# Performance work log

Hardware: AMD Instinct MI355X
Metric: run time of the kernel (lower is better)

The kernel has to match this reference:

```python
import jax, jax.numpy as jnp
import numpy as np

N_NODES = 100000


def gcn_conv(x, row, col, W, b, n_nodes):
    # PyG GCNConv: add self-loops, symmetric normalization, linear, scatter-add, bias
    deg = jnp.zeros((n_nodes,), x.dtype).at[col].add(1.0)
    dinv = jnp.where(deg > 0, jax.lax.rsqrt(deg), 0.0)
    norm = dinv[row] * dinv[col]                      # [E+N]
    h = x @ W                                         # [N, out]
    msg = h[row] * norm[:, None]                      # [E+N, out]
    out = jax.ops.segment_sum(msg, col, num_segments=n_nodes)
    return out + b


def setup_inputs() -> dict:
    key = jax.random.key(0)
    ks = jax.random.split(key, 8)
    E = 1600000
    edge_index = jax.random.randint(ks[0], (2, E), 0, N_NODES, dtype=jnp.int64)
    node_features = jax.random.normal(ks[1], (N_NODES, 16), dtype=jnp.float32)
    W1 = jax.random.normal(ks[2], (16, 32), dtype=jnp.float32) * 0.25
    b1 = jnp.zeros((32,), jnp.float32)
    W2 = jax.random.normal(ks[3], (32, 16), dtype=jnp.float32) * 0.18
    b2 = jnp.zeros((16,), jnp.float32)
    fc_W = jax.random.normal(ks[4], (16, 1), dtype=jnp.float32) * 0.25
    fc_b = jnp.zeros((1,), jnp.float32)
    return {"edge_index": edge_index, "node_features": node_features,
            "W1": W1, "b1": b1, "W2": W2, "b2": b2, "fc_W": fc_W, "fc_b": fc_b}


def reference(edge_index, node_features, W1, b1, W2, b2, fc_W, fc_b):
    n = node_features.shape[0]
    loops = jnp.arange(n, dtype=edge_index.dtype)
    row = jnp.concatenate([edge_index[0], loops])     # sources (with self-loops)
    col = jnp.concatenate([edge_index[1], loops])     # targets (with self-loops)
    x = jax.nn.relu(gcn_conv(node_features, row, col, W1, b1, n))
    # F.dropout with training=False is identity (inference)
    x = jax.nn.relu(gcn_conv(x, row, col, W2, b2, n))
    return x @ fc_W + fc_b
```

## Files before the change

kernel.cpp:

```cpp
#include <hip/hip_runtime.h>
#include <hip/hip_fp16.h>


constexpr int NN  = 100000;
constexpr int FIN = 16;
constexpr int FH  = 32;
constexpr int FO  = 16;

constexpr int BK      = 256;
constexpr int NBUCKET = (NN + BK - 1) / BK;
constexpr int CHUNK   = 8192;
constexpr int CAP     = 5376;

static __device__ __forceinline__ int pack2(float a, float b) {
    __half2 t = __float22half2_rn(make_float2(a, b));
    return *reinterpret_cast<int*>(&t);
}
static __device__ __forceinline__ float2 unpack2(int v) {
    __half2 t = *reinterpret_cast<__half2*>(&v);
    return __half22float2(t);
}

__global__ void init_kernel(int* __restrict__ bcursor) {
    int b = blockIdx.x * blockDim.x + threadIdx.x;
    if (b < NBUCKET) bcursor[b] = b * CAP;
}

__global__ __launch_bounds__(256) void bucket_fill_kernel(
        const int* __restrict__ row, const int* __restrict__ col,
        int* __restrict__ bcursor, int* __restrict__ srow, int E) {
    __shared__ int bcnt[NBUCKET];
    __shared__ int bcur[NBUCKET];
    int t = threadIdx.x;
    int e0 = blockIdx.x * CHUNK;
    int m = E - e0; if (m > CHUNK) m = CHUNK;
    for (int b = t; b < NBUCKET; b += 256) bcnt[b] = 0;
    __syncthreads();
    for (int i = t; i < m; i += 256)
        atomicAdd(&bcnt[col[e0 + i] >> 8], 1);
    __syncthreads();
    for (int b = t; b < NBUCKET; b += 256) {
        int v = bcnt[b];
        bcur[b] = v ? atomicAdd(&bcursor[b], v) : 0;
    }
    __syncthreads();
    for (int i = t; i < m; i += 256) {
        int c = col[e0 + i];
        int r = row[e0 + i];
        int p = atomicAdd(&bcur[c >> 8], 1);
        srow[p] = ((c & (BK - 1)) << 17) | r;
    }
}

__global__ __launch_bounds__(256) void bucket_sort_mm1_kernel(
        const int* __restrict__ bcursor, int* __restrict__ srow,
        int* __restrict__ off, int* __restrict__ cnt, float* __restrict__ dinv,
        const float* __restrict__ x, const float* __restrict__ W1,
        __half* __restrict__ g1, int n) {
    __shared__ int ebuf[CAP];
    __shared__ int sorted[CAP];
    __shared__ int cnt2[BK];
    __shared__ int aux[BK];
    __shared__ float w1[FIN * FH];
    int t = threadIdx.x;
    for (int i = t; i < FIN * FH; i += 256) w1[i] = W1[i];
    int lo = blockIdx.x << 8;
    int nodes = n - lo; if (nodes > BK) nodes = BK;
    int s0 = blockIdx.x * CAP;
    int m = bcursor[blockIdx.x] - s0;
    if (m > CAP) m = CAP;
    for (int i = t; i < m; i += 256) ebuf[i] = srow[s0 + i];
    cnt2[t] = 0;
    __syncthreads();
    for (int i = t; i < m; i += 256) atomicAdd(&cnt2[ebuf[i] >> 17], 1);
    __syncthreads();
    int v = cnt2[t];
    aux[t] = v;
    __syncthreads();
    for (int d = 1; d < BK; d <<= 1) {
        int a = (t >= d) ? aux[t - d] : 0;
        __syncthreads();
        aux[t] += a;
        __syncthreads();
    }
    int excl = aux[t] - v;
    cnt2[t] = excl;
    float di = rsqrtf((float)v + 1.0f);
    if (t < nodes) {
        off[lo + t]  = s0 + excl;
        cnt[lo + t]  = v;
        dinv[lo + t] = di;
    }
    __syncthreads();
    for (int i = t; i < m; i += 256) {
        int pv = ebuf[i];
        int p = atomicAdd(&cnt2[pv >> 17], 1);
        sorted[p] = pv & 0x1FFFF;
    }
    __syncthreads();
    for (int i = t; i < m; i += 256) srow[s0 + i] = sorted[i];
    if (t < nodes) {
        int nd = lo + t;
        float xi[FIN];
        const float4* xv = (const float4*)(x + (long long)nd * FIN);
        #pragma unroll
        for (int i = 0; i < FIN / 4; i++) {
            float4 vv = xv[i];
            xi[4*i] = vv.x; xi[4*i+1] = vv.y; xi[4*i+2] = vv.z; xi[4*i+3] = vv.w;
        }
        float h[FH];
        #pragma unroll
        for (int j = 0; j < FH; j++) h[j] = 0.f;
        #pragma unroll
        for (int i = 0; i < FIN; i++) {
            float xs = xi[i];
            #pragma unroll
            for (int j = 0; j < FH; j++) h[j] += xs * w1[i * FH + j];
        }
        int4* gv = (int4*)(g1 + (long long)nd * FH);
        #pragma unroll
        for (int k = 0; k < 4; k++) {
            gv[k] = make_int4(pack2(h[8*k]*di,   h[8*k+1]*di),
                              pack2(h[8*k+2]*di, h[8*k+3]*di),
                              pack2(h[8*k+4]*di, h[8*k+5]*di),
                              pack2(h[8*k+6]*di, h[8*k+7]*di));
        }
    }
}

constexpr int XS = 36;
__global__ __launch_bounds__(256) void gather_mm2_kernel(
        const int* __restrict__ off, const int* __restrict__ cnt,
        const int* __restrict__ srow, const __half* __restrict__ g1,
        const float* __restrict__ dinv, const float* __restrict__ b1,
        const float* __restrict__ W2, __half* __restrict__ g2, int n) {
    __shared__ float xs[64 * XS];
    __shared__ float w[FH * FO];
    __shared__ float bb[FH];
    int t = threadIdx.x;
    for (int i = t; i < FH * FO; i += 256) w[i] = W2[i];
    if (t < FH) bb[t] = b1[t];
    int nl = t >> 2;
    int q = t & 3;
    int node = blockIdx.x * 64 + nl;
    bool live = node < n;
    float acc[8] = {0.f,0.f,0.f,0.f,0.f,0.f,0.f,0.f};
    float di = 0.f;
    if (live) {
        di = dinv[node];
        {
            int4 raw = ((const int4*)(g1 + (long long)node * FH))[q];
            float2 f0 = unpack2(raw.x), f1 = unpack2(raw.y);
            float2 f2 = unpack2(raw.z), f3 = unpack2(raw.w);
            acc[0] = f0.x; acc[1] = f0.y; acc[2] = f1.x; acc[3] = f1.y;
            acc[4] = f2.x; acc[5] = f2.y; acc[6] = f3.x; acc[7] = f3.y;
        }
        int s = off[node];
        int m = cnt[node];
        int i = 0;
        for (; i + 3 < m; i += 4) {
            int r0 = srow[s + i];
            int r1 = srow[s + i + 1];
            int r2 = srow[s + i + 2];
            int r3 = srow[s + i + 3];
            int4 ra = ((const int4*)(g1 + (long long)r0 * FH))[q];
            int4 rb = ((const int4*)(g1 + (long long)r1 * FH))[q];
            int4 rc = ((const int4*)(g1 + (long long)r2 * FH))[q];
            int4 rd = ((const int4*)(g1 + (long long)r3 * FH))[q];
            float2 u;
            u = unpack2(ra.x); acc[0] += u.x; acc[1] += u.y;
            u = unpack2(ra.y); acc[2] += u.x; acc[3] += u.y;
            u = unpack2(ra.z); acc[4] += u.x; acc[5] += u.y;
            u = unpack2(ra.w); acc[6] += u.x; acc[7] += u.y;
            u = unpack2(rb.x); acc[0] += u.x; acc[1] += u.y;
            u = unpack2(rb.y); acc[2] += u.x; acc[3] += u.y;
            u = unpack2(rb.z); acc[4] += u.x; acc[5] += u.y;
            u = unpack2(rb.w); acc[6] += u.x; acc[7] += u.y;
            u = unpack2(rc.x); acc[0] += u.x; acc[1] += u.y;
            u = unpack2(rc.y); acc[2] += u.x; acc[3] += u.y;
            u = unpack2(rc.z); acc[4] += u.x; acc[5] += u.y;
            u = unpack2(rc.w); acc[6] += u.x; acc[7] += u.y;
            u = unpack2(rd.x); acc[0] += u.x; acc[1] += u.y;
            u = unpack2(rd.y); acc[2] += u.x; acc[3] += u.y;
            u = unpack2(rd.z); acc[4] += u.x; acc[5] += u.y;
            u = unpack2(rd.w); acc[6] += u.x; acc[7] += u.y;
        }
        for (; i < m; i++) {
            int r0 = srow[s + i];
            int4 ra = ((const int4*)(g1 + (long long)r0 * FH))[q];
            float2 u;
            u = unpack2(ra.x); acc[0] += u.x; acc[1] += u.y;
            u = unpack2(ra.y); acc[2] += u.x; acc[3] += u.y;
            u = unpack2(ra.z); acc[4] += u.x; acc[5] += u.y;
            u = unpack2(ra.w); acc[6] += u.x; acc[7] += u.y;
        }
    }
    __syncthreads();
    if (live) {
        float* xr = xs + nl * XS + 8 * q;
        #pragma unroll
        for (int j = 0; j < 8; j++) {
            float a = acc[j] * di + bb[8*q + j];
            xr[j] = a > 0.f ? a : 0.f;
        }
    }
    __syncthreads();
    if (live) {
        const float* xr = xs + nl * XS;
        int k0 = 4 * q;
        float o0 = 0.f, o1 = 0.f, o2 = 0.f, o3 = 0.f;
        #pragma unroll
        for (int j = 0; j < FH; j++) {
            float xj = xr[j];
            const float* wr = w + j * FO + k0;
            o0 += xj * wr[0];
            o1 += xj * wr[1];
            o2 += xj * wr[2];
            o3 += xj * wr[3];
        }
        ((int2*)(g2 + (long long)node * FO))[q] =
            make_int2(pack2(o0 * di, o1 * di), pack2(o2 * di, o3 * di));
    }
}

__global__ __launch_bounds__(256) void gather_fc_kernel(
        const int* __restrict__ off, const int* __restrict__ cnt,
        const int* __restrict__ srow, const __half* __restrict__ g2,
        const float* __restrict__ dinv, const float* __restrict__ b2,
        const float* __restrict__ fcW, const float* __restrict__ fcb,
        float* __restrict__ out, int n) {
    __shared__ float w[FO];
    __shared__ float bb[FO];
    __shared__ float fb;
    int t = threadIdx.x;
    if (t < FO) { w[t] = fcW[t]; bb[t] = b2[t]; }
    if (t == 0) fb = fcb[0];
    __syncthreads();
    int node = blockIdx.x * 128 + (t >> 1);
    int q = t & 1;
    if (node >= n) return;
    float di = dinv[node];
    float acc[8];
    {
        int4 raw = ((const int4*)(g2 + (long long)node * FO))[q];
        float2 f0 = unpack2(raw.x), f1 = unpack2(raw.y);
        float2 f2 = unpack2(raw.z), f3 = unpack2(raw.w);
        acc[0] = f0.x; acc[1] = f0.y; acc[2] = f1.x; acc[3] = f1.y;
        acc[4] = f2.x; acc[5] = f2.y; acc[6] = f3.x; acc[7] = f3.y;
    }
    int s = off[node];
    int m = cnt[node];
    int i = 0;
    for (; i + 3 < m; i += 4) {
        int r0 = srow[s + i];
        int r1 = srow[s + i + 1];
        int r2 = srow[s + i + 2];
        int r3 = srow[s + i + 3];
        int4 ra = ((const int4*)(g2 + (long long)r0 * FO))[q];
        int4 rb = ((const int4*)(g2 + (long long)r1 * FO))[q];
        int4 rc = ((const int4*)(g2 + (long long)r2 * FO))[q];
        int4 rd = ((const int4*)(g2 + (long long)r3 * FO))[q];
        float2 u;
        u = unpack2(ra.x); acc[0] += u.x; acc[1] += u.y;
        u = unpack2(ra.y); acc[2] += u.x; acc[3] += u.y;
        u = unpack2(ra.z); acc[4] += u.x; acc[5] += u.y;
        u = unpack2(ra.w); acc[6] += u.x; acc[7] += u.y;
        u = unpack2(rb.x); acc[0] += u.x; acc[1] += u.y;
        u = unpack2(rb.y); acc[2] += u.x; acc[3] += u.y;
        u = unpack2(rb.z); acc[4] += u.x; acc[5] += u.y;
        u = unpack2(rb.w); acc[6] += u.x; acc[7] += u.y;
        u = unpack2(rc.x); acc[0] += u.x; acc[1] += u.y;
        u = unpack2(rc.y); acc[2] += u.x; acc[3] += u.y;
        u = unpack2(rc.z); acc[4] += u.x; acc[5] += u.y;
        u = unpack2(rc.w); acc[6] += u.x; acc[7] += u.y;
        u = unpack2(rd.x); acc[0] += u.x; acc[1] += u.y;
        u = unpack2(rd.y); acc[2] += u.x; acc[3] += u.y;
        u = unpack2(rd.z); acc[4] += u.x; acc[5] += u.y;
        u = unpack2(rd.w); acc[6] += u.x; acc[7] += u.y;
    }
    for (; i < m; i++) {
        int r0 = srow[s + i];
        int4 ra = ((const int4*)(g2 + (long long)r0 * FO))[q];
        float2 u;
        u = unpack2(ra.x); acc[0] += u.x; acc[1] += u.y;
        u = unpack2(ra.y); acc[2] += u.x; acc[3] += u.y;
        u = unpack2(ra.z); acc[4] += u.x; acc[5] += u.y;
        u = unpack2(ra.w); acc[6] += u.x; acc[7] += u.y;
    }
    float p = 0.f;
    #pragma unroll
    for (int j = 0; j < 8; j++) {
        float a = acc[j] * di + bb[8*q + j];
        p += (a > 0.f ? a : 0.f) * w[8*q + j];
    }
    p += __shfl_down(p, 1, 2);
    if (q == 0) out[node] = p + fb;
}

extern "C" void kernel_launch(void* const* d_in, const int* in_sizes, int n_in,
                              void* d_out, int out_size, void* d_ws, size_t ws_size,
                              hipStream_t stream) {
    const int*   edge = (const int*)d_in[0];
    const float* x    = (const float*)d_in[1];
    const float* W1   = (const float*)d_in[2];
    const float* b1   = (const float*)d_in[3];
    const float* W2   = (const float*)d_in[4];
    const float* b2   = (const float*)d_in[5];
    const float* fcW  = (const float*)d_in[6];
    const float* fcb  = (const float*)d_in[7];
    float* out = (float*)d_out;

    const int E = in_sizes[0] / 2;
    const int n = NN;
    const int* row = edge;
    const int* col = edge + E;

    const size_t nA = (size_t)((n + 127) & ~127);
    char* wsb = (char*)d_ws;
    int*   cnt     = (int*)wsb;
    int*   off     = cnt + nA;
    float* dinv    = (float*)(off + nA);
    int*   bcursor = (int*)(dinv + nA);
    int*   srow    = bcursor + 512;
    int*   srowEnd = srow + (size_t)(NBUCKET + 1) * CAP;
    __half* g1     = (__half*)srowEnd;
    __half* g2     = g1 + (size_t)n * FH;

    const int B = 256;
    const int nChunkBlocks = (E + CHUNK - 1) / CHUNK;

    init_kernel<<<2, B, 0, stream>>>(bcursor);
    bucket_fill_kernel<<<nChunkBlocks, B, 0, stream>>>(row, col, bcursor, srow, E);
    bucket_sort_mm1_kernel<<<NBUCKET, B, 0, stream>>>(bcursor, srow, off, cnt, dinv, x, W1, g1, n);
    gather_mm2_kernel<<<(n + 63) / 64, B, 0, stream>>>(off, cnt, srow, g1, dinv, b1, W2, g2, n);
    gather_fc_kernel<<<(n + 127) / 128, B, 0, stream>>>(off, cnt, srow, g2, dinv, b2, fcW, fcb, out, n);
}
```

Measured before the change: 151.2 us.

## Pack offset/count into int2, drop shared edge buffer, halve fill chunk size

Merges the per-node offset and count arrays into one int2 array, so the gather kernels do one 8-byte load instead of two separate loads. Removes the shared-memory staging buffer in the bucket sort kernel and reads srow from global memory twice instead, which lowers LDS use and may raise occupancy. Halves CHUNK so bucket_fill launches twice as many blocks, trading more global atomics on bucket cursors for more parallelism.

```diff
diff --git a/kernel.cpp b/kernel.cpp
--- a/kernel.cpp
+++ b/kernel.cpp
@@ -9,7 +9,7 @@
 
 constexpr int BK      = 256;
 constexpr int NBUCKET = (NN + BK - 1) / BK;
-constexpr int CHUNK   = 8192;
+constexpr int CHUNK   = 4096;
 constexpr int CAP     = 5376;
 
 static __device__ __forceinline__ int pack2(float a, float b) {
@@ -54,10 +54,9 @@
 
 __global__ __launch_bounds__(256) void bucket_sort_mm1_kernel(
         const int* __restrict__ bcursor, int* __restrict__ srow,
-        int* __restrict__ off, int* __restrict__ cnt, float* __restrict__ dinv,
+        int2* __restrict__ offcnt, float* __restrict__ dinv,
         const float* __restrict__ x, const float* __restrict__ W1,
         __half* __restrict__ g1, int n) {
-    __shared__ int ebuf[CAP];
     __shared__ int sorted[CAP];
     __shared__ int cnt2[BK];
     __shared__ int aux[BK];
@@ -69,10 +68,9 @@
     int s0 = blockIdx.x * CAP;
     int m = bcursor[blockIdx.x] - s0;
     if (m > CAP) m = CAP;
-    for (int i = t; i < m; i += 256) ebuf[i] = srow[s0 + i];
     cnt2[t] = 0;
     __syncthreads();
-    for (int i = t; i < m; i += 256) atomicAdd(&cnt2[ebuf[i] >> 17], 1);
+    for (int i = t; i < m; i += 256) atomicAdd(&cnt2[srow[s0 + i] >> 17], 1);
     __syncthreads();
     int v = cnt2[t];
     aux[t] = v;
@@ -87,13 +85,12 @@
     cnt2[t] = excl;
     float di = rsqrtf((float)v + 1.0f);
     if (t < nodes) {
-        off[lo + t]  = s0 + excl;
-        cnt[lo + t]  = v;
-        dinv[lo + t] = di;
+        offcnt[lo + t] = make_int2(s0 + excl, v);
+        dinv[lo + t]   = di;
     }
     __syncthreads();
     for (int i = t; i < m; i += 256) {
-        int pv = ebuf[i];
+        int pv = srow[s0 + i];
         int p = atomicAdd(&cnt2[pv >> 17], 1);
         sorted[p] = pv & 0x1FFFF;
     }
@@ -130,7 +127,7 @@
 
 constexpr int XS = 36;
 __global__ __launch_bounds__(256) void gather_mm2_kernel(
-        const int* __restrict__ off, const int* __restrict__ cnt,
+        const int2* __restrict__ offcnt,
         const int* __restrict__ srow, const __half* __restrict__ g1,
         const float* __restrict__ dinv, const float* __restrict__ b1,
         const float* __restrict__ W2, __half* __restrict__ g2, int n) {
@@ -155,8 +152,8 @@
             acc[0] = f0.x; acc[1] = f0.y; acc[2] = f1.x; acc[3] = f1.y;
             acc[4] = f2.x; acc[5] = f2.y; acc[6] = f3.x; acc[7] = f3.y;
         }
-        int s = off[node];
-        int m = cnt[node];
+        int2 oc = offcnt[node];
+        int s = oc.x, m = oc.y;
         int i = 0;
         for (; i + 3 < m; i += 4) {
             int r0 = srow[s + i];
@@ -224,7 +221,7 @@
 }
 
 __global__ __launch_bounds__(256) void gather_fc_kernel(
-        const int* __restrict__ off, const int* __restrict__ cnt,
+        const int2* __restrict__ offcnt,
         const int* __restrict__ srow, const __half* __restrict__ g2,
         const float* __restrict__ dinv, const float* __restrict__ b2,
         const float* __restrict__ fcW, const float* __restrict__ fcb,
@@ -248,8 +245,8 @@
         acc[0] = f0.x; acc[1] = f0.y; acc[2] = f1.x; acc[3] = f1.y;
         acc[4] = f2.x; acc[5] = f2.y; acc[6] = f3.x; acc[7] = f3.y;
     }
-    int s = off[node];
-    int m = cnt[node];
+    int2 oc = offcnt[node];
+    int s = oc.x, m = oc.y;
     int i = 0;
     for (; i + 3 < m; i += 4) {
         int r0 = srow[s + i];
@@ -317,9 +314,8 @@
 
     const size_t nA = (size_t)((n + 127) & ~127);
     char* wsb = (char*)d_ws;
-    int*   cnt     = (int*)wsb;
-    int*   off     = cnt + nA;
-    float* dinv    = (float*)(off + nA);
+    int2*  offcnt  = (int2*)wsb;
+    float* dinv    = (float*)(offcnt + nA);
     int*   bcursor = (int*)(dinv + nA);
     int*   srow    = bcursor + 512;
     int*   srowEnd = srow + (size_t)(NBUCKET + 1) * CAP;
@@ -331,7 +327,7 @@
 
     init_kernel<<<2, B, 0, stream>>>(bcursor);
     bucket_fill_kernel<<<nChunkBlocks, B, 0, stream>>>(row, col, bcursor, srow, E);
-    bucket_sort_mm1_kernel<<<NBUCKET, B, 0, stream>>>(bcursor, srow, off, cnt, dinv, x, W1, g1, n);
-    gather_mm2_kernel<<<(n + 63) / 64, B, 0, stream>>>(off, cnt, srow, g1, dinv, b1, W2, g2, n);
-    gather_fc_kernel<<<(n + 127) / 128, B, 0, stream>>>(off, cnt, srow, g2, dinv, b2, fcW, fcb, out, n);
-}
+    bucket_sort_mm1_kernel<<<NBUCKET, B, 0, stream>>>(bcursor, srow, offcnt, dinv, x, W1, g1, n);
+    gather_mm2_kernel<<<(n + 63) / 64, B, 0, stream>>>(offcnt, srow, g1, dinv, b1, W2, g2, n);
+    gather_fc_kernel<<<(n + 127) / 128, B, 0, stream>>>(offcnt, srow, g2, dinv, b2, fcW, fcb, out, n);
+}
```

After: 156.1 us. 1.03x slower.
